# Kernel optimization log

Measured on AMD Instinct MI355X. Metric: run time of the kernel, lower is better.

Reference implementation:

```python
import jax, jax.numpy as jnp
import numpy as np

N, FIN, FOUT = 4096, 256, 256


def setup_inputs() -> dict:
    key = jax.random.key(0)
    ks = jax.random.split(key, 6)
    x = jax.random.normal(ks[0], (N, FIN), jnp.float32)
    adj = jax.random.randint(ks[1], (N, N), 0, 2, jnp.int32)  # dense 0/1 adjacency
    W = jax.random.normal(ks[2], (FOUT, FIN), jnp.float32) / np.sqrt(FIN)
    b = jax.random.normal(ks[3], (FOUT,), jnp.float32) * 0.01
    att_w = jax.random.normal(ks[4], (2 * FOUT,), jnp.float32) / np.sqrt(2.0 * FOUT)  # Linear(2F,1).weight squeezed
    att_b = jax.random.normal(ks[5], (), jnp.float32) * 0.01
    return {"x": x, "adj": adj, "W": W, "b": b, "att_w": att_w, "att_b": att_b}


def reference(x, adj, W, b, att_w, att_b):
    n = x.shape[0]
    fo = W.shape[0]
    h = x @ W.T + b  # [N, Fout]
    # score(i,j) = att([h_i ; h_j]) = h_i.w1 + h_j.w2 + att_b  -> no [N,N,2F] concat
    s = (h @ att_w[:fo])[:, None] + (h @ att_w[fo:])[None, :] + att_b  # [N, N]
    edge = adj == 1
    # GLOBAL softmax over all edges (faithful to F.softmax(stacked_scores, dim=0))
    gmax = jnp.max(jnp.where(edge, s, -jnp.inf))
    e = jnp.exp(s - gmax)
    denom = jnp.sum(jnp.where(edge, e, 0.0))
    p = (e / denom).reshape(-1)  # softmaxed score per pair (valid at edges)
    # original indexes attention_scores[j] by NODE id j into the row-major edge list:
    # recover the score of the j-th global edge (j = 0..N-1) via cumsum rank + scatter
    flat = edge.reshape(-1)
    rank = jnp.cumsum(flat.astype(jnp.int32)) - 1  # rank of each edge in row-major order
    idx = jnp.where(flat, rank, n)  # non-edges and ranks >= n get dropped
    w_node = jnp.zeros((n,), h.dtype).at[idx].set(p, mode="drop")  # [N]
    # output[i] = sum_{j: adj[i,j]==1} w_node[j] * h[j]
    out = jax.nn.relu(edge.astype(h.dtype) @ (w_node[:, None] * h))
    return out
```

## Files before the change

### kernel.cpp

```cpp
#include <hip/hip_runtime.h>
#include <cstdint>
#include <cstddef>

#define NN 4096
#define FDIM 256

typedef __attribute__((ext_vector_type(4))) float fx4;
typedef __attribute__((ext_vector_type(2))) float fx2;
typedef __attribute__((ext_vector_type(8))) short s8v;

__device__ inline uint16_t f2bf(float f) {
    union { float f; uint32_t u; } v; v.f = f;
    uint32_t u = v.u;
    uint32_t r = (u + 0x7FFFu + ((u >> 16) & 1u)) >> 16;
    return (uint16_t)r;
}

__global__ __launch_bounds__(512) void k_h(const float* __restrict__ x,
        const float* __restrict__ W, const float* __restrict__ bias,
        const float* __restrict__ att_w, float* __restrict__ h,
        float* __restrict__ a1p, float* __restrict__ a2p) {
    __shared__ __align__(16) float xs[2][64 * 68];
    __shared__ __align__(16) float wt[2][64 * 68];
    const int bi = blockIdx.x, bf = blockIdx.y;
    const int t = threadIdx.x;
    const int t256 = t & 255;
    const int kh = t >> 8;
    const int tx = t256 & 15, ty = t256 >> 4;
    float acc[4][4] = {};
    float rx[8], rw[8];
    #pragma unroll
    for (int u = 0; u < 8; ++u) {
        const int e = t + 512 * u, r = e >> 6, c = e & 63;
        rx[u] = x[(size_t)(bi * 64 + r) * 256 + c];
        rw[u] = W[(size_t)(bf * 64 + r) * 256 + c];
    }
    for (int p = 0; p < 4; ++p) {
        float* xb = xs[p & 1];
        float* wb = wt[p & 1];
        #pragma unroll
        for (int u = 0; u < 8; ++u) {
            const int e = t + 512 * u, r = e >> 6, c = e & 63;
            const int sw = 8 * ((c & 7) ^ ((c >> 3) & 7));
            xb[c * 68 + (r ^ sw)] = rx[u];
            wb[c * 68 + (r ^ sw)] = rw[u];
        }
        __syncthreads();
        if (p < 3) {
            const int k0 = (p + 1) * 64;
            #pragma unroll
            for (int u = 0; u < 8; ++u) {
                const int e = t + 512 * u, r = e >> 6, c = e & 63;
                rx[u] = x[(size_t)(bi * 64 + r) * 256 + k0 + c];
                rw[u] = W[(size_t)(bf * 64 + r) * 256 + k0 + c];
            }
        }
        #pragma unroll 8
        for (int k = 0; k < 32; ++k) {
            const int kk = kh * 32 + k;
            const int sw = 8 * ((kk & 7) ^ ((kk >> 3) & 7));
            const fx4 av = *(const fx4*)(xb + kk * 68 + ((ty * 4) ^ sw));
            const fx4 bv = *(const fx4*)(wb + kk * 68 + ((tx * 4) ^ sw));
            #pragma unroll
            for (int u = 0; u < 4; ++u)
                #pragma unroll
                for (int v = 0; v < 4; ++v)
                    acc[u][v] += av[u] * bv[v];
        }
    }
    __syncthreads();
    float* cbuf = xs[0];
    if (kh == 1) {
        #pragma unroll
        for (int u = 0; u < 4; ++u)
            *(fx4*)(cbuf + t256 * 16 + u * 4) = *(const fx4*)(&acc[u][0]);
    }
    __syncthreads();
    if (kh == 0) {
        #pragma unroll
        for (int u = 0; u < 4; ++u) {
            const fx4 o = *(const fx4*)(cbuf + t256 * 16 + u * 4);
            #pragma unroll
            for (int v = 0; v < 4; ++v) acc[u][v] += o[v];
        }
        const fx4 bv = *(const fx4*)(bias + bf * 64 + tx * 4);
        const fx4 w1v = *(const fx4*)(att_w + bf * 64 + tx * 4);
        const fx4 w2v = *(const fx4*)(att_w + 256 + bf * 64 + tx * 4);
        #pragma unroll
        for (int u = 0; u < 4; ++u) {
            const int i = bi * 64 + ty * 4 + u;
            fx4 r;
            float s1 = 0.f, s2 = 0.f;
            #pragma unroll
            for (int v = 0; v < 4; ++v) {
                r[v] = acc[u][v] + bv[v];
                s1 += r[v] * w1v[v];
                s2 += r[v] * w2v[v];
            }
            *(fx4*)(h + (size_t)i * 256 + bf * 64 + tx * 4) = r;
            #pragma unroll
            for (int d = 8; d > 0; d >>= 1) {
                s1 += __shfl_down(s1, d, 16);
                s2 += __shfl_down(s2, d, 16);
            }
            if (tx == 0) {
                a1p[bf * NN + i] = s1;
                a2p[bf * NN + i] = s2;
            }
        }
    }
}

__global__ __launch_bounds__(1024) void k_prep(const float* __restrict__ a1p,
        const float* __restrict__ a2p, const int* __restrict__ adj,
        float* __restrict__ E1, float* __restrict__ E2,
        float* __restrict__ wraw, float* __restrict__ Sg) {
    __shared__ float E1s[NN];
    __shared__ float E2s[NN];
    __shared__ float red1[16], red2[16];
    __shared__ int wtot[16];
    __shared__ int base_s;
    const int t = threadIdx.x, lane = t & 63, wv = t >> 6;
    fx4 v1 = {0.f, 0.f, 0.f, 0.f}, v2 = {0.f, 0.f, 0.f, 0.f};
    #pragma unroll
    for (int bf = 0; bf < 4; ++bf) {
        v1 += *(const fx4*)(a1p + bf * NN + t * 4);
        v2 += *(const fx4*)(a2p + bf * NN + t * 4);
    }
    float m1 = fmaxf(fmaxf(v1[0], v1[1]), fmaxf(v1[2], v1[3]));
    float m2 = fmaxf(fmaxf(v2[0], v2[1]), fmaxf(v2[2], v2[3]));
    #pragma unroll
    for (int d = 32; d > 0; d >>= 1) {
        m1 = fmaxf(m1, __shfl_down(m1, d));
        m2 = fmaxf(m2, __shfl_down(m2, d));
    }
    if (lane == 0) { red1[wv] = m1; red2[wv] = m2; }
    __syncthreads();
    if (t == 0) {
        float mm1 = -1e30f, mm2 = -1e30f;
        for (int k = 0; k < 16; ++k) {
            mm1 = fmaxf(mm1, red1[k]);
            mm2 = fmaxf(mm2, red2[k]);
        }
        red1[0] = mm1; red2[0] = mm2;
        *Sg = 0.f;
        base_s = 0;
    }
    __syncthreads();
    const float M1 = red1[0], M2 = red2[0];
    fx4 e1v, e2v, z4 = {0.f, 0.f, 0.f, 0.f};
    #pragma unroll
    for (int j = 0; j < 4; ++j) {
        e1v[j] = expf(v1[j] - M1);
        e2v[j] = expf(v2[j] - M2);
    }
    *(fx4*)(E1s + t * 4) = e1v;
    *(fx4*)(E2s + t * 4) = e2v;
    *(fx4*)(E1 + t * 4) = e1v;
    *(fx4*)(E2 + t * 4) = e2v;
    *(fx4*)(wraw + t * 4) = z4;
    __syncthreads();
    for (int row = 0; row < NN; ++row) {
        const int base = base_s;
        if (base >= NN) break;
        const int4 a = ((const int4*)(adj + (size_t)row * NN))[t];
        const int vj[4] = {a.x, a.y, a.z, a.w};
        int cnt = 0;
        #pragma unroll
        for (int j = 0; j < 4; ++j) cnt += (vj[j] == 1);
        int inc = cnt;
        #pragma unroll
        for (int d = 1; d < 64; d <<= 1) {
            const int y = __shfl_up(inc, d);
            if (lane >= d) inc += y;
        }
        if (lane == 63) wtot[wv] = inc;
        __syncthreads();
        int wbase = 0, total = 0;
        #pragma unroll
        for (int w = 0; w < 16; ++w) {
            const int xw = wtot[w];
            total += xw;
            wbase += (w < wv) ? xw : 0;
        }
        if (t == 0) base_s = base + total;
        int r = base + wbase + inc - cnt;
        if (cnt && r < NN) {
            const float e1 = E1s[row];
            #pragma unroll
            for (int j = 0; j < 4; ++j) {
                if (vj[j] == 1) {
                    if (r < NN) wraw[r] = e1 * E2s[t * 4 + j];
                    ++r;
                }
            }
        }
        __syncthreads();
    }
}

__global__ __launch_bounds__(256) void k_g(const float* __restrict__ h,
        const float* __restrict__ wraw, uint16_t* __restrict__ gt) {
    __shared__ float tile[64 * 33];
    const int bj = blockIdx.x, bf = blockIdx.y;
    const int j0 = bj * 64, f0 = bf * 32;
    const int t = threadIdx.x;
    #pragma unroll
    for (int p = 0; p < 8; ++p) {
        const int e = t + 256 * p;
        const int jl = e >> 5, fl = e & 31;
        tile[jl * 33 + fl] = h[(size_t)(j0 + jl) * 256 + f0 + fl] * wraw[j0 + jl];
    }
    __syncthreads();
    {
        const int fl = t >> 3, cb = t & 7;
        const int phys_cb = cb ^ (fl & 7);
        s8v v;
        #pragma unroll
        for (int lo = 0; lo < 8; ++lo)
            v[lo] = (short)f2bf(tile[(cb * 8 + lo) * 33 + fl]);
        *(s8v*)(gt + (size_t)(f0 + fl) * NN + j0 + phys_cb * 8) = v;
    }
}

__global__ __launch_bounds__(256) void k_fused(const int* __restrict__ adj,
        const uint16_t* __restrict__ gt, const float* __restrict__ E1,
        const float* __restrict__ E2, uint16_t* __restrict__ part,
        float* __restrict__ Sg, int krange) {
    __shared__ __align__(16) uint16_t As[64 * 72];
    __shared__ __align__(16) uint16_t Gs[256 * 64];
    __shared__ __align__(16) uint16_t GsS[16 * 72];
    const int ib = blockIdx.x, ks = blockIdx.y;
    const int t = threadIdx.x;
    const int wv = t >> 6, lane = t & 63;
    const int q = lane >> 4, m16 = lane & 15;
    const int i0 = ib * 64, k0 = ks * krange;
    const int ksteps = krange >> 6;
    fx4 acc[4][4];
    #pragma unroll
    for (int a = 0; a < 4; ++a)
        #pragma unroll
        for (int b = 0; b < 4; ++b) acc[a][b] = (fx4){0.f, 0.f, 0.f, 0.f};
    fx4 accS[4];
    #pragma unroll
    for (int a = 0; a < 4; ++a) accS[a] = (fx4){0.f, 0.f, 0.f, 0.f};
    for (int e = t; e < 15 * 72; e += 256) GsS[72 + e] = 0;

    const int fr = lane >> 3, cb = lane & 7;
    const int ar = t >> 4, ac4 = (t & 15) * 4;
    int4 ra[4];
    #pragma unroll
    for (int p = 0; p < 4; ++p)
        ra[p] = *(const int4*)(adj + (size_t)(i0 + p * 16 + ar) * NN + k0 + ac4);

    for (int step = 0; step < ksteps; ++step) {
        const int kk = k0 + step * 64;
        #pragma unroll
        for (int p = 0; p < 4; ++p) {
            uint2 w;
            w.x = (uint32_t)(ra[p].x | (ra[p].y << 16)) * 0x3F80u;
            w.y = (uint32_t)(ra[p].z | (ra[p].w << 16)) * 0x3F80u;
            *(uint2*)(&As[(p * 16 + ar) * 72 + ac4]) = w;
        }
        #pragma unroll
        for (int p = 0; p < 8; ++p) {
            const int f0 = wv * 64 + p * 8;
            const uint16_t* gp = gt + (size_t)(f0 + fr) * NN + kk + cb * 8;
            __builtin_amdgcn_global_load_lds(
                (const __attribute__((address_space(1))) uint32_t*)gp,
                (__attribute__((address_space(3))) uint32_t*)(Gs + f0 * 64),
                16, 0, 0);
        }
        if (t < 8) {
            const float* e2p = E2 + kk + t * 8;
            uint32_t* dst = (uint32_t*)(&GsS[t * 8]);
            #pragma unroll
            for (int j = 0; j < 4; ++j)
                dst[j] = (uint32_t)f2bf(e2p[2 * j]) |
                         ((uint32_t)f2bf(e2p[2 * j + 1]) << 16);
        }
        __syncthreads();
        if (step + 1 < ksteps) {
            #pragma unroll
            for (int p = 0; p < 4; ++p)
                ra[p] = *(const int4*)(adj + (size_t)(i0 + p * 16 + ar) * NN +
                                       kk + 64 + ac4);
        }
        s8v afr[4][2];
        #pragma unroll
        for (int it = 0; it < 4; ++it)
            #pragma unroll
            for (int kh = 0; kh < 2; ++kh)
                afr[it][kh] = *(const s8v*)(As + (it * 16 + m16) * 72 + kh * 32 + q * 8);
        #pragma unroll
        for (int ft = 0; ft < 4; ++ft) {
            #pragma unroll
            for (int kh = 0; kh < 2; ++kh) {
                const int row = wv * 64 + ft * 16 + m16;
                const int pcb = ((kh << 2) | q) ^ (m16 & 7);
                const s8v bfr = *(const s8v*)(Gs + row * 64 + pcb * 8);
                #pragma unroll
                for (int it = 0; it < 4; ++it)
                    acc[it][ft] = __builtin_amdgcn_mfma_f32_16x16x32_bf16(
                        afr[it][kh], bfr, acc[it][ft], 0, 0, 0);
            }
        }
        if (wv == 3) {
            #pragma unroll
            for (int kh = 0; kh < 2; ++kh) {
                const s8v bfrS = *(const s8v*)(GsS + m16 * 72 + kh * 32 + q * 8);
                #pragma unroll
                for (int it = 0; it < 4; ++it)
                    accS[it] = __builtin_amdgcn_mfma_f32_16x16x32_bf16(
                        afr[it][kh], bfrS, accS[it], 0, 0, 0);
            }
        }
        __syncthreads();
    }
    if (wv == 3) {
        float s_local = 0.f;
        #pragma unroll
        for (int it = 0; it < 4; ++it)
            #pragma unroll
            for (int r = 0; r < 4; ++r)
                s_local += accS[it][r] * E1[i0 + it * 16 + q * 4 + r];
        #pragma unroll
        for (int d = 32; d > 0; d >>= 1) s_local += __shfl_down(s_local, d);
        if (lane == 0) atomicAdd(Sg, s_local);
    }
    uint16_t* dst = part + (size_t)ks * NN * FDIM;
    #pragma unroll
    for (int it = 0; it < 4; ++it) {
        #pragma unroll
        for (int ft = 0; ft < 4; ++ft) {
            const int f = wv * 64 + ft * 16 + m16;
            #pragma unroll
            for (int r = 0; r < 4; ++r) {
                const int i = i0 + it * 16 + q * 4 + r;
                dst[(size_t)i * FDIM + f] = f2bf(acc[it][ft][r]);
            }
        }
    }
}

__global__ __launch_bounds__(256) void k_out(const uint16_t* __restrict__ part,
        const float* __restrict__ Sg, float* __restrict__ out, int nsplit) {
    const size_t idx = ((size_t)blockIdx.x * 256 + threadIdx.x) * 8;
    const float inv = 1.0f / (*Sg);
    float s[8] = {};
    for (int k = 0; k < nsplit; ++k) {
        const s8v v = *(const s8v*)(part + (size_t)k * NN * FDIM + idx);
        #pragma unroll
        for (int j = 0; j < 8; ++j) {
            union { uint32_t u; float f; } cv;
            cv.u = ((uint32_t)(uint16_t)v[j]) << 16;
            s[j] += cv.f;
        }
    }
    fx4 r0, r1;
    #pragma unroll
    for (int j = 0; j < 4; ++j) {
        r0[j] = fmaxf(s[j], 0.f) * inv;
        r1[j] = fmaxf(s[4 + j], 0.f) * inv;
    }
    *(fx4*)(out + idx) = r0;
    *(fx4*)(out + idx + 4) = r1;
}

extern "C" void kernel_launch(void* const* d_in, const int* in_sizes, int n_in,
                              void* d_out, int out_size, void* d_ws, size_t ws_size,
                              hipStream_t stream) {
    const float* x     = (const float*)d_in[0];
    const int*   adj   = (const int*)d_in[1];
    const float* W     = (const float*)d_in[2];
    const float* bias  = (const float*)d_in[3];
    const float* att_w = (const float*)d_in[4];
    float* out = (float*)d_out;
    char* ws = (char*)d_ws;
    float*    h    = (float*)(ws + 0);
    uint16_t* gt   = (uint16_t*)(ws + (size_t)4194304);
    float*    a1p  = (float*)(ws + 6291456);
    float*    a2p  = (float*)(ws + 6356992);
    float*    E1   = (float*)(ws + 6422528);
    float*    E2   = (float*)(ws + 6438912);
    float*    wraw = (float*)(ws + 6455296);
    float*    Sg   = (float*)(ws + 6471680);
    uint16_t* part = (uint16_t*)(ws + 6471936);

    const size_t avail = (ws_size > 6471936) ? (ws_size - 6471936) : 0;
    int splitk = 1;
    while (splitk < 8 &&
           (size_t)(splitk * 2) * NN * FDIM * sizeof(uint16_t) <= avail)
        splitk <<= 1;
    const int krange = NN / splitk;

    k_h    <<<dim3(64, 4), 512, 0, stream>>>(x, W, bias, att_w, h, a1p, a2p);
    k_prep <<<dim3(1), 1024, 0, stream>>>(a1p, a2p, adj, E1, E2, wraw, Sg);
    k_g    <<<dim3(64, 8), 256, 0, stream>>>(h, wraw, gt);
    k_fused<<<dim3(64, splitk), 256, 0, stream>>>(adj, gt, E1, E2, part, Sg, krange);
    k_out  <<<dim3(512), 256, 0, stream>>>(part, Sg, out, splitk);
}
```

Measured before the change: 146.0 us.

## Fuse transpose-to-bf16 into linear kernel and fold node weights into adjacency tile

Removes the separate k_g kernel. The linear kernel now writes h directly as transposed bf16 through a shared-memory tile, and the per-node weight wraw moves into the adjacency A operand of the fused matmul instead of being applied to h. The denominator sum is now computed with scalar FMAs on adjacency values already in registers, replacing the extra MFMA path on one wave. The aim is to save a kernel launch, the fp32 h round trip through memory, and MFMA work, at the cost of rounding wraw to bf16 inside A, which changes numerics.

```diff
diff --git a/kernel.cpp b/kernel.cpp
--- a/kernel.cpp
+++ b/kernel.cpp
@@ -6,19 +6,17 @@
 #define FDIM 256
 
 typedef __attribute__((ext_vector_type(4))) float fx4;
-typedef __attribute__((ext_vector_type(2))) float fx2;
 typedef __attribute__((ext_vector_type(8))) short s8v;
 
 __device__ inline uint16_t f2bf(float f) {
     union { float f; uint32_t u; } v; v.f = f;
-    uint32_t u = v.u;
-    uint32_t r = (u + 0x7FFFu + ((u >> 16) & 1u)) >> 16;
-    return (uint16_t)r;
-}
-
-__global__ __launch_bounds__(512) void k_h(const float* __restrict__ x,
+    const uint32_t u = v.u;
+    return (uint16_t)((u + 0x7FFFu + ((u >> 16) & 1u)) >> 16);
+}
+
+__global__ __launch_bounds__(512, 4) void k_h(const float* __restrict__ x,
         const float* __restrict__ W, const float* __restrict__ bias,
-        const float* __restrict__ att_w, float* __restrict__ h,
+        const float* __restrict__ att_w, uint16_t* __restrict__ gt,
         float* __restrict__ a1p, float* __restrict__ a2p) {
     __shared__ __align__(16) float xs[2][64 * 68];
     __shared__ __align__(16) float wt[2][64 * 68];
@@ -47,12 +45,12 @@
         }
         __syncthreads();
         if (p < 3) {
-            const int k0 = (p + 1) * 64;
+            const int kc = (p + 1) * 64;
             #pragma unroll
             for (int u = 0; u < 8; ++u) {
                 const int e = t + 512 * u, r = e >> 6, c = e & 63;
-                rx[u] = x[(size_t)(bi * 64 + r) * 256 + k0 + c];
-                rw[u] = W[(size_t)(bf * 64 + r) * 256 + k0 + c];
+                rx[u] = x[(size_t)(bi * 64 + r) * 256 + kc + c];
+                rw[u] = W[(size_t)(bf * 64 + r) * 256 + kc + c];
             }
         }
         #pragma unroll 8
@@ -77,6 +75,7 @@
     }
     __syncthreads();
     if (kh == 0) {
+        float* tileT = wt[0];
         #pragma unroll
         for (int u = 0; u < 4; ++u) {
             const fx4 o = *(const fx4*)(cbuf + t256 * 16 + u * 4);
@@ -97,7 +96,9 @@
                 s1 += r[v] * w1v[v];
                 s2 += r[v] * w2v[v];
             }
-            *(fx4*)(h + (size_t)i * 256 + bf * 64 + tx * 4) = r;
+            #pragma unroll
+            for (int v = 0; v < 4; ++v)
+                tileT[(tx * 4 + v) * 68 + ty * 4 + u] = r[v];
             #pragma unroll
             for (int d = 8; d > 0; d >>= 1) {
                 s1 += __shfl_down(s1, d, 16);
@@ -108,6 +109,17 @@
                 a2p[bf * NN + i] = s2;
             }
         }
+    }
+    __syncthreads();
+    {
+        const float* tileT = wt[0];
+        const int fl = t >> 3, cb = t & 7;
+        const int pcb = cb ^ (fl & 7);
+        s8v v;
+        #pragma unroll
+        for (int lo = 0; lo < 8; ++lo)
+            v[lo] = (short)f2bf(tileT[fl * 68 + cb * 8 + lo]);
+        *(s8v*)(gt + (size_t)(bf * 64 + fl) * NN + bi * 64 + pcb * 8) = v;
     }
 }
 
@@ -199,68 +211,53 @@
     }
 }
 
-__global__ __launch_bounds__(256) void k_g(const float* __restrict__ h,
-        const float* __restrict__ wraw, uint16_t* __restrict__ gt) {
-    __shared__ float tile[64 * 33];
-    const int bj = blockIdx.x, bf = blockIdx.y;
-    const int j0 = bj * 64, f0 = bf * 32;
-    const int t = threadIdx.x;
-    #pragma unroll
-    for (int p = 0; p < 8; ++p) {
-        const int e = t + 256 * p;
-        const int jl = e >> 5, fl = e & 31;
-        tile[jl * 33 + fl] = h[(size_t)(j0 + jl) * 256 + f0 + fl] * wraw[j0 + jl];
-    }
-    __syncthreads();
-    {
-        const int fl = t >> 3, cb = t & 7;
-        const int phys_cb = cb ^ (fl & 7);
-        s8v v;
-        #pragma unroll
-        for (int lo = 0; lo < 8; ++lo)
-            v[lo] = (short)f2bf(tile[(cb * 8 + lo) * 33 + fl]);
-        *(s8v*)(gt + (size_t)(f0 + fl) * NN + j0 + phys_cb * 8) = v;
-    }
-}
-
-__global__ __launch_bounds__(256) void k_fused(const int* __restrict__ adj,
+__global__ __launch_bounds__(256, 3) void k_fused(const int* __restrict__ adj,
         const uint16_t* __restrict__ gt, const float* __restrict__ E1,
-        const float* __restrict__ E2, uint16_t* __restrict__ part,
-        float* __restrict__ Sg, int krange) {
+        const float* __restrict__ E2, const float* __restrict__ wraw,
+        uint16_t* __restrict__ part, float* __restrict__ Sg, int krange) {
     __shared__ __align__(16) uint16_t As[64 * 72];
     __shared__ __align__(16) uint16_t Gs[256 * 64];
-    __shared__ __align__(16) uint16_t GsS[16 * 72];
+    __shared__ float sgred[4];
     const int ib = blockIdx.x, ks = blockIdx.y;
     const int t = threadIdx.x;
     const int wv = t >> 6, lane = t & 63;
     const int q = lane >> 4, m16 = lane & 15;
     const int i0 = ib * 64, k0 = ks * krange;
     const int ksteps = krange >> 6;
+    const int ar = t >> 4, ac4 = (t & 15) * 4;
+    const int fr = lane >> 3, cb = lane & 7;
     fx4 acc[4][4];
     #pragma unroll
     for (int a = 0; a < 4; ++a)
         #pragma unroll
-        for (int b = 0; b < 4; ++b) acc[a][b] = (fx4){0.f, 0.f, 0.f, 0.f};
-    fx4 accS[4];
-    #pragma unroll
-    for (int a = 0; a < 4; ++a) accS[a] = (fx4){0.f, 0.f, 0.f, 0.f};
-    for (int e = t; e < 15 * 72; e += 256) GsS[72 + e] = 0;
-
-    const int fr = lane >> 3, cb = lane & 7;
-    const int ar = t >> 4, ac4 = (t & 15) * 4;
+        for (int b2 = 0; b2 < 4; ++b2) acc[a][b2] = (fx4){0.f, 0.f, 0.f, 0.f};
+    float sS = 0.f;
+    float e1r[4];
+    #pragma unroll
+    for (int p = 0; p < 4; ++p) e1r[p] = E1[i0 + p * 16 + ar];
     int4 ra[4];
     #pragma unroll
     for (int p = 0; p < 4; ++p)
         ra[p] = *(const int4*)(adj + (size_t)(i0 + p * 16 + ar) * NN + k0 + ac4);
-
-    for (int step = 0; step < ksteps; ++step) {
-        const int kk = k0 + step * 64;
+    fx4 rw4 = *(const fx4*)(wraw + k0 + ac4);
+    fx4 re2 = *(const fx4*)(E2 + k0 + ac4);
+
+    for (int stp = 0; stp < ksteps; ++stp) {
+        const int kk = k0 + stp * 64;
+        const uint16_t wb0 = f2bf(rw4[0]), wb1 = f2bf(rw4[1]);
+        const uint16_t wb2 = f2bf(rw4[2]), wb3 = f2bf(rw4[3]);
         #pragma unroll
         for (int p = 0; p < 4; ++p) {
-            uint2 w;
-            w.x = (uint32_t)(ra[p].x | (ra[p].y << 16)) * 0x3F80u;
-            w.y = (uint32_t)(ra[p].z | (ra[p].w << 16)) * 0x3F80u;
-            *(uint2*)(&As[(p * 16 + ar) * 72 + ac4]) = w;
+            uint2 wo;
+            wo.x = (ra[p].x == 1 ? (uint32_t)wb0 : 0u) |
+                   ((ra[p].y == 1 ? (uint32_t)wb1 : 0u) << 16);
+            wo.y = (ra[p].z == 1 ? (uint32_t)wb2 : 0u) |
+                   ((ra[p].w == 1 ? (uint32_t)wb3 : 0u) << 16);
+            *(uint2*)(&As[(p * 16 + ar) * 72 + ac4]) = wo;
+            sS += e1r[p] * ((ra[p].x == 1 ? re2[0] : 0.f) +
+                            (ra[p].y == 1 ? re2[1] : 0.f) +
+                            (ra[p].z == 1 ? re2[2] : 0.f) +
+                            (ra[p].w == 1 ? re2[3] : 0.f));
         }
         #pragma unroll
         for (int p = 0; p < 8; ++p) {
@@ -271,63 +268,42 @@
                 (__attribute__((address_space(3))) uint32_t*)(Gs + f0 * 64),
                 16, 0, 0);
         }
-        if (t < 8) {
-            const float* e2p = E2 + kk + t * 8;
-            uint32_t* dst = (uint32_t*)(&GsS[t * 8]);
-            #pragma unroll
-            for (int j = 0; j < 4; ++j)
-                dst[j] = (uint32_t)f2bf(e2p[2 * j]) |
-                         ((uint32_t)f2bf(e2p[2 * j + 1]) << 16);
-        }
-        __syncthreads();
-        if (step + 1 < ksteps) {
+        __syncthreads();
+        if (stp + 1 < ksteps) {
             #pragma unroll
             for (int p = 0; p < 4; ++p)
                 ra[p] = *(const int4*)(adj + (size_t)(i0 + p * 16 + ar) * NN +
                                        kk + 64 + ac4);
+            rw4 = *(const fx4*)(wraw + kk + 64 + ac4);
+            re2 = *(const fx4*)(E2 + kk + 64 + ac4);
         }
         s8v afr[4][2];
         #pragma unroll
         for (int it = 0; it < 4; ++it)
             #pragma unroll
-            for (int kh = 0; kh < 2; ++kh)
-                afr[it][kh] = *(const s8v*)(As + (it * 16 + m16) * 72 + kh * 32 + q * 8);
+            for (int khh = 0; khh < 2; ++khh)
+                afr[it][khh] = *(const s8v*)(As + (it * 16 + m16) * 72 + khh * 32 + q * 8);
         #pragma unroll
         for (int ft = 0; ft < 4; ++ft) {
             #pragma unroll
-            for (int kh = 0; kh < 2; ++kh) {
+            for (int khh = 0; khh < 2; ++khh) {
                 const int row = wv * 64 + ft * 16 + m16;
-                const int pcb = ((kh << 2) | q) ^ (m16 & 7);
+                const int pcb = ((khh << 2) | q) ^ (m16 & 7);
                 const s8v bfr = *(const s8v*)(Gs + row * 64 + pcb * 8);
                 #pragma unroll
                 for (int it = 0; it < 4; ++it)
                     acc[it][ft] = __builtin_amdgcn_mfma_f32_16x16x32_bf16(
-                        afr[it][kh], bfr, acc[it][ft], 0, 0, 0);
-            }
-        }
-        if (wv == 3) {
-            #pragma unroll
-            for (int kh = 0; kh < 2; ++kh) {
-                const s8v bfrS = *(const s8v*)(GsS + m16 * 72 + kh * 32 + q * 8);
-                #pragma unroll
-                for (int it = 0; it < 4; ++it)
-                    accS[it] = __builtin_amdgcn_mfma_f32_16x16x32_bf16(
-                        afr[it][kh], bfrS, accS[it], 0, 0, 0);
-            }
-        }
-        __syncthreads();
-    }
-    if (wv == 3) {
-        float s_local = 0.f;
-        #pragma unroll
-        for (int it = 0; it < 4; ++it)
-            #pragma unroll
-            for (int r = 0; r < 4; ++r)
-                s_local += accS[it][r] * E1[i0 + it * 16 + q * 4 + r];
-        #pragma unroll
-        for (int d = 32; d > 0; d >>= 1) s_local += __shfl_down(s_local, d);
-        if (lane == 0) atomicAdd(Sg, s_local);
-    }
+                        afr[it][khh], bfr, acc[it][ft], 0, 0, 0);
+            }
+        }
+        __syncthreads();
+    }
+    #pragma unroll
+    for (int d = 32; d > 0; d >>= 1) sS += __shfl_down(sS, d);
+    if (lane == 0) sgred[wv] = sS;
+    __syncthreads();
+    if (t == 0)
+        atomicAdd(Sg, sgred[0] + sgred[1] + sgred[2] + sgred[3]);
     uint16_t* dst = part + (size_t)ks * NN * FDIM;
     #pragma unroll
     for (int it = 0; it < 4; ++it) {
@@ -377,26 +353,25 @@
     const float* att_w = (const float*)d_in[4];
     float* out = (float*)d_out;
     char* ws = (char*)d_ws;
-    float*    h    = (float*)(ws + 0);
-    uint16_t* gt   = (uint16_t*)(ws + (size_t)4194304);
-    float*    a1p  = (float*)(ws + 6291456);
-    float*    a2p  = (float*)(ws + 6356992);
-    float*    E1   = (float*)(ws + 6422528);
-    float*    E2   = (float*)(ws + 6438912);
-    float*    wraw = (float*)(ws + 6455296);
-    float*    Sg   = (float*)(ws + 6471680);
-    uint16_t* part = (uint16_t*)(ws + 6471936);
-
-    const size_t avail = (ws_size > 6471936) ? (ws_size - 6471936) : 0;
+    uint16_t* gt   = (uint16_t*)(ws + 0);
+    float*    a1p  = (float*)(ws + 2097152);
+    float*    a2p  = (float*)(ws + 2162688);
+    float*    E1   = (float*)(ws + 2228224);
+    float*    E2   = (float*)(ws + 2244608);
+    float*    wraw = (float*)(ws + 2260992);
+    float*    Sg   = (float*)(ws + 2277376);
+    uint16_t* part = (uint16_t*)(ws + 2277632);
+    (void)in_sizes; (void)n_in; (void)out_size;
+
+    const size_t avail = (ws_size > 2277632) ? (ws_size - 2277632) : 0;
     int splitk = 1;
     while (splitk < 8 &&
            (size_t)(splitk * 2) * NN * FDIM * sizeof(uint16_t) <= avail)
         splitk <<= 1;
     const int krange = NN / splitk;
 
-    k_h    <<<dim3(64, 4), 512, 0, stream>>>(x, W, bias, att_w, h, a1p, a2p);
+    k_h    <<<dim3(64, 4), 512, 0, stream>>>(x, W, bias, att_w, gt, a1p, a2p);
     k_prep <<<dim3(1), 1024, 0, stream>>>(a1p, a2p, adj, E1, E2, wraw, Sg);
-    k_g    <<<dim3(64, 8), 256, 0, stream>>>(h, wraw, gt);
-    k_fused<<<dim3(64, splitk), 256, 0, stream>>>(adj, gt, E1, E2, part, Sg, krange);
+    k_fused<<<dim3(64, splitk), 256, 0, stream>>>(adj, gt, E1, E2, wraw, part, Sg, krange);
     k_out  <<<dim3(512), 256, 0, stream>>>(part, Sg, out, splitk);
 }
```

New measurement: 148.1 us. Within noise of the previous version (+1.4%).
